# Performance work log

Hardware: AMD Instinct MI355X
Metric: run time of the kernel (lower is better)

The kernel has to match this reference:

```python
import jax, jax.numpy as jnp
from jax import lax
import numpy as np

B, N, C = 32, 24564, 81
CENTER_VAR, SIZE_VAR = 0.1, 0.2
CONF_THRESH, IOU_THRESH = 0.01, 0.45
PRE_NMS_K, MAX_DET = 100, 100
EPS = 1e-8


def setup_inputs() -> dict:
    key = jax.random.key(0)
    k1, k2, k3, k4 = jax.random.split(key, 4)
    location_preds = jax.random.normal(k1, (B, N, 4), dtype=jnp.float32)
    confidence_preds = jax.random.normal(k2, (B, N, C), dtype=jnp.float32)
    # priors in center form (cx, cy, w, h), all in (0, 1), w/h in [0.05, 0.5]
    cxcy = jax.random.uniform(k3, (N, 2), dtype=jnp.float32)
    wh = 0.05 + 0.45 * jax.random.uniform(k4, (N, 2), dtype=jnp.float32)
    priors = jnp.concatenate([cxcy, wh], axis=-1)
    return {"location_preds": location_preds,
            "confidence_preds": confidence_preds,
            "priors": priors}


def _decode_corner(loc, priors):
    # loc: [B,N,4], priors: [N,4] center form -> corner-form boxes [B,N,4]
    cxcy = loc[..., :2] * CENTER_VAR * priors[None, :, 2:] + priors[None, :, :2]
    wh = jnp.exp(loc[..., 2:] * SIZE_VAR) * priors[None, :, 2:]
    return jnp.concatenate([cxcy - wh * 0.5, cxcy + wh * 0.5], axis=-1)


def _pairwise_iou(boxes):
    # boxes: [K,4] corner form -> [K,K]
    lt = jnp.maximum(boxes[:, None, :2], boxes[None, :, :2])
    rb = jnp.minimum(boxes[:, None, 2:], boxes[None, :, 2:])
    wh = jnp.clip(rb - lt, 0.0)
    inter = wh[..., 0] * wh[..., 1]
    area = jnp.prod(jnp.clip(boxes[:, 2:] - boxes[:, :2], 0.0), axis=-1)  # [K]
    return inter / (area[:, None] + area[None, :] - inter + EPS)


def _nms_one_class(boxes, scores):
    # boxes: [N,4], scores: [N] -> kept top-K boxes/scores for this class
    scores = jnp.where(scores > CONF_THRESH, scores, 0.0)
    top_s, idx = lax.top_k(scores, PRE_NMS_K)          # [K]
    top_b = boxes[idx]                                  # [K,4] sorted by score desc
    iou = _pairwise_iou(top_b)                          # [K,K]
    order = jnp.arange(PRE_NMS_K)

    def body(i, keep):
        suppressed = jnp.any(keep & (iou[:, i] > IOU_THRESH) & (order < i))
        return keep.at[i].set((top_s[i] > 0.0) & jnp.logical_not(suppressed))

    keep = lax.fori_loop(0, PRE_NMS_K, body, jnp.zeros(PRE_NMS_K, dtype=bool))
    return top_b, jnp.where(keep, top_s, 0.0)


def _per_image(boxes, scores):
    # boxes: [N,4], scores: [N,C]; class 0 is background
    cls_scores = scores[:, 1:].T                        # [C-1, N]
    b, s = jax.vmap(_nms_one_class, in_axes=(None, 0))(boxes, cls_scores)
    labels = jnp.broadcast_to(jnp.arange(1, C)[:, None], (C - 1, PRE_NMS_K))
    b = b.reshape(-1, 4)
    s = s.reshape(-1)
    labels = labels.reshape(-1)
    top_s, idx = lax.top_k(s, MAX_DET)
    return b[idx], top_s, labels[idx]


def reference(location_preds, confidence_preds, priors):
    scores = jax.nn.softmax(confidence_preds, axis=2)   # [B,N,C]
    bboxes = _decode_corner(location_preds, priors)     # [B,N,4]
    boxes_out, scores_out, labels_out = jax.vmap(_per_image)(bboxes, scores)
    # boxes_out [B,MAX_DET,4], scores_out [B,MAX_DET], labels_out [B,MAX_DET]
    return boxes_out, scores_out, labels_out
```

## Files before the change

kernel.cpp:

```cpp
#include <hip/hip_runtime.h>
#include <cstdint>
#include <cstddef>

#define BB 32
#define NN 24564
#define CC 81
#define CM1 80
#define KTOP 100
#define MAXDET 100
#define CBINS 28
#define CSHIFT 21
#define BASEBITS 0x3C000000u
#define SPECBITS 0x3D400000u
#define SPECPF   0.0468281f
#define CAP2 2048
#define CAPB 25
#define BPI 96
#define CAPS 1024
#define FCH 8
#define FCHN 1000
#define FPAD 1024
#define NCAND (CM1 * KTOP)

typedef unsigned long long ull;
typedef unsigned int uint;
typedef float floatx4 __attribute__((ext_vector_type(4)));
typedef floatx4 uf4 __attribute__((aligned(4)));

__global__ __launch_bounds__(256) void zero_kernel(uint* __restrict__ p, int nwords) {
    int i = blockIdx.x * 256 + threadIdx.x;
    if (i < nwords) p[i] = 0u;
}

__device__ __forceinline__ void bitonic_sort256(ull* a, int S, int tid) {
    for (int k = 2; k <= S; k <<= 1) {
        for (int j = k >> 1; j > 0; j >>= 1) {
            for (int i = tid; i < S; i += 256) {
                int ixj = i ^ j;
                if (ixj > i) {
                    ull x = a[i], y = a[ixj];
                    bool up = ((i & k) == 0);
                    if ((x > y) == up) { a[i] = y; a[ixj] = x; }
                }
            }
            __syncthreads();
        }
    }
}

__global__ __launch_bounds__(256) void softmax_spec_kernel(const float* __restrict__ conf,
                                                           float2* __restrict__ mxs,
                                                           ull* __restrict__ cand,
                                                           uint* __restrict__ ccnt,
                                                           uint* __restrict__ ovf) {
    __shared__ ull  sbuf[CM1 * CAPB];
    __shared__ uint scnt[CM1];
    int tid = threadIdx.x;
    if (tid < CM1) scnt[tid] = 0u;
    __syncthreads();

    int b = blockIdx.x / BPI, j = blockIdx.x % BPI;
    int n = j * 256 + tid;
    if (n < NN) {
        const float* row = conf + ((size_t)b * NN + n) * CC;
        const uf4* row4 = reinterpret_cast<const uf4*>(row);
        float r[CC];
        #pragma unroll
        for (int q = 0; q < 20; ++q) {
            floatx4 v = row4[q];
            r[4 * q] = v.x; r[4 * q + 1] = v.y; r[4 * q + 2] = v.z; r[4 * q + 3] = v.w;
        }
        r[80] = row[80];

        float mx = r[0];
        #pragma unroll
        for (int c = 1; c < CC; ++c) mx = fmaxf(mx, r[c]);

        float s = 0.f;
        #pragma unroll
        for (int c = 0; c < CC; ++c) {
            r[c] = expf(__fsub_rn(r[c], mx));
            s = __fadd_rn(s, r[c]);
        }
        mxs[(size_t)b * NN + n] = make_float2(mx, s);

        float rcp = __builtin_amdgcn_rcpf(s);
        uint nn = (uint)n;
        #pragma unroll
        for (int c = 1; c < CC; ++c) {
            float p = __fmul_rn(r[c], rcp);
            if (p > SPECPF) {
                float sc = __fdiv_rn(r[c], s);
                uint eb = __float_as_uint(sc);
                if (eb >= SPECBITS) {
                    uint pp = atomicAdd(&scnt[c - 1], 1u);
                    if (pp < CAPB) sbuf[(c - 1) * CAPB + pp] = (((ull)(~eb)) << 32) | nn;
                }
            }
        }
    }
    __syncthreads();

    if (tid < CM1) {
        uint c2 = scnt[tid];
        if (c2) {
            int bc = b * CM1 + tid;
            uint nstore = c2 > CAPB ? CAPB : c2;
            uint base = atomicAdd(ccnt + bc, nstore);
            if (c2 > CAPB || base + nstore > CAP2) ovf[bc] = 1u;
            uint lim = base + nstore; if (lim > CAP2) lim = CAP2;
            for (uint i = 0; base + i < lim; ++i)
                cand[(size_t)bc * CAP2 + base + i] = sbuf[tid * CAPB + i];
        }
    }
}

__global__ __launch_bounds__(256) void nms_kernel(const ull* __restrict__ cand,
                                                  const uint* __restrict__ ccnt,
                                                  const uint* __restrict__ ovf,
                                                  const float* __restrict__ conf,
                                                  const float2* __restrict__ mxs,
                                                  const float* __restrict__ loc,
                                                  const float* __restrict__ priors,
                                                  float* __restrict__ nms_scores,
                                                  float* __restrict__ nms_boxes) {
    int bc = blockIdx.x;
    int bimg = bc / CM1, ccls = bc % CM1;
    __shared__ ull arr[CAP2];
    __shared__ ull arr2[CAPS];
    __shared__ uint hist[CBINS];
    __shared__ uint s_cut, s_mode, s_cnt2;
    __shared__ float bx[KTOP][4];
    __shared__ float sv[KTOP];
    __shared__ ull mlo[KTOP], mhi[KTOP];
    __shared__ ull keeplo, keephi;

    int tid = threadIdx.x;
    for (int i = tid; i < CBINS; i += 256) hist[i] = 0u;
    if (tid == 0) { s_cut = 0u; s_mode = 0u; s_cnt2 = 0u; }
    __syncthreads();

    uint rawcnt = ccnt[bc];
    bool flagged = !(ovf[bc] == 0u && rawcnt >= (uint)KTOP);
    int scc; ull* sorted;

    if (!flagged) {
        int cc = (int)rawcnt; if (cc > CAP2) cc = CAP2;
        const ull* crow = cand + (size_t)bc * CAP2;
        for (int i = tid; i < cc; i += 256) {
            ull k = crow[i];
            arr[i] = k;
            uint bits = ~(uint)(k >> 32);
            uint bin = (bits - BASEBITS) >> CSHIFT;
            if (bin >= CBINS) bin = CBINS - 1;
            atomicAdd(&hist[bin], 1u);
        }
        __syncthreads();
        if (tid == 0) {
            uint Kt = (uint)(cc < KTOP ? cc : KTOP);
            if (Kt > 0) {
                uint cum = 0; int bb2 = 0;
                for (int i = CBINS - 1; i >= 0; --i) {
                    cum += hist[i];
                    if (cum >= Kt) { bb2 = i; break; }
                }
                if (cum <= CAPS) {
                    s_cut = BASEBITS + ((uint)bb2 << CSHIFT);
                    s_mode = 1u;
                }
            }
        }
        __syncthreads();
        if (s_mode) {
            uint cutv = s_cut;
            for (int i = tid; i < cc; i += 256) {
                ull k = arr[i];
                uint bits = ~(uint)(k >> 32);
                if (bits >= cutv) { uint p = atomicAdd(&s_cnt2, 1u); arr2[p] = k; }
            }
            __syncthreads();
            scc = (int)s_cnt2;
            sorted = arr2;
        } else {
            scc = cc;
            sorted = arr;
        }
    } else {
        int c = ccls + 1;
        for (int n = tid; n < NN; n += 256) {
            float x = conf[((size_t)bimg * NN + n) * CC + c];
            float2 ms = mxs[(size_t)bimg * NN + n];
            float e = expf(__fsub_rn(x, ms.x));
            float sc = __fdiv_rn(e, ms.y);
            if (sc > 0.01f) {
                uint bits = __float_as_uint(sc);
                uint bin = (bits - BASEBITS) >> CSHIFT;
                if (bin >= CBINS) bin = CBINS - 1;
                atomicAdd(&hist[bin], 1u);
            }
        }
        __syncthreads();
        if (tid == 0) {
            uint total = 0;
            for (int i = 0; i < CBINS; ++i) total += hist[i];
            uint Kt = total < KTOP ? total : KTOP;
            s_cut = 0xFFFFFFFFu;
            if (Kt > 0) {
                uint cum = 0; int bb2 = 0;
                for (int i = CBINS - 1; i >= 0; --i) {
                    cum += hist[i];
                    if (cum >= Kt) { bb2 = i; break; }
                }
                uint cutbin = (cum <= CAP2) ? (uint)bb2 : (uint)(bb2 + 1);
                s_cut = BASEBITS + (cutbin << CSHIFT);
            }
        }
        __syncthreads();
        uint cutv = s_cut;
        for (int n = tid; n < NN; n += 256) {
            float x = conf[((size_t)bimg * NN + n) * CC + c];
            float2 ms = mxs[(size_t)bimg * NN + n];
            float e = expf(__fsub_rn(x, ms.x));
            float sc = __fdiv_rn(e, ms.y);
            if (sc > 0.01f) {
                uint bits = __float_as_uint(sc);
                if (bits >= cutv) {
                    uint p = atomicAdd(&s_cnt2, 1u);
                    if (p < CAP2) arr[p] = (((ull)(~bits)) << 32) | (uint)n;
                }
            }
        }
        __syncthreads();
        scc = (int)s_cnt2; if (scc > CAP2) scc = CAP2;
        sorted = arr;
    }

    int S = 1; while (S < scc) S <<= 1; if (S < 2) S = 2;
    for (int i = scc + tid; i < S; i += 256) sorted[i] = ~0ull;
    __syncthreads();
    bitonic_sort256(sorted, S, tid);

    if (tid < KTOP) {
        float val = 0.f; uint n = 0;
        if (tid < scc) {
            ull kk = sorted[tid];
            val = __uint_as_float(~(uint)(kk >> 32));
            n = (uint)(kk & 0xFFFFFFFFu);
        }
        sv[tid] = val;
        float4 l = reinterpret_cast<const float4*>(loc)[(size_t)bimg * NN + n];
        float4 p = reinterpret_cast<const float4*>(priors)[n];
        float cx = __fadd_rn(__fmul_rn(__fmul_rn(l.x, 0.1f), p.z), p.x);
        float cy = __fadd_rn(__fmul_rn(__fmul_rn(l.y, 0.1f), p.w), p.y);
        float w  = __fmul_rn(expf(__fmul_rn(l.z, 0.2f)), p.z);
        float h  = __fmul_rn(expf(__fmul_rn(l.w, 0.2f)), p.w);
        bx[tid][0] = __fsub_rn(cx, __fmul_rn(w, 0.5f));
        bx[tid][1] = __fsub_rn(cy, __fmul_rn(h, 0.5f));
        bx[tid][2] = __fadd_rn(cx, __fmul_rn(w, 0.5f));
        bx[tid][3] = __fadd_rn(cy, __fmul_rn(h, 0.5f));
    }
    __syncthreads();

    if (tid < KTOP) {
        float x1 = bx[tid][0], y1 = bx[tid][1], x2 = bx[tid][2], y2 = bx[tid][3];
        float ai = __fmul_rn(fmaxf(__fsub_rn(x2, x1), 0.f), fmaxf(__fsub_rn(y2, y1), 0.f));
        ull lo = 0, hi = 0;
        for (int jj = 0; jj < KTOP; ++jj) {
            float jx1 = bx[jj][0], jy1 = bx[jj][1], jx2 = bx[jj][2], jy2 = bx[jj][3];
            float iw = fmaxf(__fsub_rn(fminf(x2, jx2), fmaxf(x1, jx1)), 0.f);
            float ih = fmaxf(__fsub_rn(fminf(y2, jy2), fmaxf(y1, jy1)), 0.f);
            float inter = __fmul_rn(iw, ih);
            float aj = __fmul_rn(fmaxf(__fsub_rn(jx2, jx1), 0.f), fmaxf(__fsub_rn(jy2, jy1), 0.f));
            float denom = __fadd_rn(__fsub_rn(__fadd_rn(ai, aj), inter), 1e-8f);
            float iou = __fdiv_rn(inter, denom);
            if (iou > 0.45f) { if (jj < 64) lo |= (1ull << jj); else hi |= (1ull << (jj - 64)); }
        }
        mlo[tid] = lo; mhi[tid] = hi;
    }
    __syncthreads();

    if (tid == 0) {
        ull klo = 0, khi = 0;
        for (int i = 0; i < KTOP; ++i) {
            ull sup = (mlo[i] & klo) | (mhi[i] & khi);
            bool kp = (sv[i] > 0.f) && (sup == 0ull);
            if (kp) { if (i < 64) klo |= (1ull << i); else khi |= (1ull << (i - 64)); }
        }
        keeplo = klo; keephi = khi;
    }
    __syncthreads();

    if (tid < KTOP) {
        bool kp = (tid < 64) ? ((keeplo >> tid) & 1ull) : ((keephi >> (tid - 64)) & 1ull);
        size_t obase = (size_t)bc * KTOP + tid;
        nms_scores[obase] = kp ? sv[tid] : 0.f;
        float4 o; o.x = bx[tid][0]; o.y = bx[tid][1]; o.z = bx[tid][2]; o.w = bx[tid][3];
        reinterpret_cast<float4*>(nms_boxes)[obase] = o;
    }
}

__global__ __launch_bounds__(256) void final_topk_kernel(const float* __restrict__ nms_scores,
                                                         const float* __restrict__ nms_boxes,
                                                         float* __restrict__ out) {
    int b = blockIdx.x;
    __shared__ ull arr[CAP2];
    __shared__ ull arr2[FPAD];
    __shared__ uint hist[CBINS];
    __shared__ uint s_cut, s_mode, s_cnt2, s_nz;
    int tid = threadIdx.x;

    const float* srow = nms_scores + (size_t)b * NCAND;
    for (int i = tid; i < CBINS; i += 256) hist[i] = 0u;
    if (tid == 0) { s_cut = 0u; s_mode = 0u; s_cnt2 = 0u; s_nz = 0u; }
    __syncthreads();

    uint mynz = 0;
    for (int i = tid; i < NCAND; i += 256) {
        float s = srow[i];
        if (s > 0.f) {
            ++mynz;
            uint bits = __float_as_uint(s);
            uint bin = (bits - BASEBITS) >> CSHIFT;
            if (bin >= CBINS) bin = CBINS - 1;
            atomicAdd(&hist[bin], 1u);
        }
    }
    if (mynz) atomicAdd(&s_nz, mynz);
    __syncthreads();
    if (tid == 0) {
        if (s_nz >= (uint)KTOP) {
            uint cum = 0; int bb2 = 0;
            for (int i = CBINS - 1; i >= 0; --i) {
                cum += hist[i];
                if (cum >= (uint)KTOP) { bb2 = i; break; }
            }
            if (cum <= CAP2) { s_cut = BASEBITS + ((uint)bb2 << CSHIFT); s_mode = 1u; }
        }
    }
    __syncthreads();

    if (s_mode) {
        uint cutv = s_cut;
        for (int i = tid; i < NCAND; i += 256) {
            float s = srow[i];
            if (s > 0.f) {
                uint bits = __float_as_uint(s);
                if (bits >= cutv) {
                    uint p = atomicAdd(&s_cnt2, 1u);
                    arr[p] = (((ull)(~bits)) << 32) | (uint)i;
                }
            }
        }
        __syncthreads();
        int fcc = (int)s_cnt2;
        int FS = 1; while (FS < fcc) FS <<= 1; if (FS < 2) FS = 2;
        for (int i = fcc + tid; i < FS; i += 256) arr[i] = ~0ull;
        __syncthreads();
        bitonic_sort256(arr, FS, tid);
    } else {
        for (int ch = 0; ch < FCH; ++ch) {
            for (int i = tid; i < FPAD; i += 256) {
                ull key;
                if (i < FCHN) {
                    float s = srow[ch * FCHN + i];
                    uint bits = (s > 0.f) ? __float_as_uint(s) : 0u;
                    key = (((ull)(~bits)) << 32) | (uint)(ch * FCHN + i);
                } else key = ~0ull;
                arr2[i] = key;
            }
            __syncthreads();
            bitonic_sort256(arr2, FPAD, tid);
            if (tid < KTOP) arr[ch * KTOP + tid] = arr2[tid];
            __syncthreads();
        }
        for (int i = FCH * KTOP + tid; i < FPAD; i += 256) arr[i] = ~0ull;
        __syncthreads();
        bitonic_sort256(arr, FPAD, tid);
    }

    if (tid < MAXDET) {
        ull kk = arr[tid];
        uint hb = (uint)(kk >> 32);
        uint idx = (uint)(kk & 0xFFFFFFFFu);
        float val = __uint_as_float(~hb);
        float4 b4 = reinterpret_cast<const float4*>(nms_boxes)[(size_t)b * NCAND + idx];
        reinterpret_cast<float4*>(out)[(size_t)b * MAXDET + tid] = b4;
        out[BB * MAXDET * 4 + b * MAXDET + tid] = val;
        out[BB * MAXDET * 5 + b * MAXDET + tid] = (float)(idx / KTOP + 1);
    }
}

extern "C" void kernel_launch(void* const* d_in, const int* in_sizes, int n_in,
                              void* d_out, int out_size, void* d_ws, size_t ws_size,
                              hipStream_t stream) {
    const float* loc    = (const float*)d_in[0];
    const float* conf   = (const float*)d_in[1];
    const float* priors = (const float*)d_in[2];
    float* out = (float*)d_out;

    char* ws = (char*)d_ws;
    float* nms_scores = (float*)ws;
    float* nms_boxes  = nms_scores + (size_t)BB * CM1 * KTOP;
    ull*   cand       = (ull*)(nms_boxes + (size_t)BB * CM1 * KTOP * 4);
    float2* mxs       = (float2*)(cand + (size_t)BB * CM1 * CAP2);
    uint*  ccnt       = (uint*)(mxs + (size_t)BB * NN);
    uint*  ovf        = ccnt + (size_t)BB * CM1;

    zero_kernel<<<(BB * CM1 * 2 + 255) / 256, 256, 0, stream>>>(ccnt, BB * CM1 * 2);

    softmax_spec_kernel<<<BB * BPI, 256, 0, stream>>>(conf, mxs, cand, ccnt, ovf);
    nms_kernel<<<BB * CM1, 256, 0, stream>>>(cand, ccnt, ovf, conf, mxs, loc, priors,
                                             nms_scores, nms_boxes);
    final_topk_kernel<<<BB, 256, 0, stream>>>(nms_scores, nms_boxes, out);
}
```

Baseline: 234.4 us.

## Replace bitonic sort with rank-by-counting top-K selection in NMS kernel

Drops the shared-memory copy of candidates and the bitonic sort. Each thread instead computes the rank of up to 8 keys by comparing against all surviving candidates and scatters those with rank below K into a top-K buffer. The fallback path that kept all candidates when the post-cut count exceeded the old cap is removed, so the cut filter is always applied. This avoids the many barrier-separated sort stages, but the ranking costs O(scc) serial shared reads per thread, which can grow when many candidates survive the cut.

```diff
diff --git a/kernel.cpp b/kernel.cpp
--- a/kernel.cpp
+++ b/kernel.cpp
@@ -16,7 +16,6 @@
 #define CAP2 2048
 #define CAPB 25
 #define BPI 96
-#define CAPS 1024
 #define FCH 8
 #define FCHN 1000
 #define FPAD 1024
@@ -126,10 +125,10 @@
                                                   float* __restrict__ nms_boxes) {
     int bc = blockIdx.x;
     int bimg = bc / CM1, ccls = bc % CM1;
-    __shared__ ull arr[CAP2];
-    __shared__ ull arr2[CAPS];
+    __shared__ ull arr2[CAP2];
+    __shared__ ull keysort[KTOP];
     __shared__ uint hist[CBINS];
-    __shared__ uint s_cut, s_mode, s_cnt2;
+    __shared__ uint s_cut, s_cnt2;
     __shared__ float bx[KTOP][4];
     __shared__ float sv[KTOP];
     __shared__ ull mlo[KTOP], mhi[KTOP];
@@ -137,20 +136,18 @@
 
     int tid = threadIdx.x;
     for (int i = tid; i < CBINS; i += 256) hist[i] = 0u;
-    if (tid == 0) { s_cut = 0u; s_mode = 0u; s_cnt2 = 0u; }
+    if (tid < KTOP) keysort[tid] = ((ull)0xFFFFFFFFu) << 32;
+    if (tid == 0) { s_cut = 0u; s_cnt2 = 0u; }
     __syncthreads();
 
     uint rawcnt = ccnt[bc];
     bool flagged = !(ovf[bc] == 0u && rawcnt >= (uint)KTOP);
-    int scc; ull* sorted;
 
     if (!flagged) {
         int cc = (int)rawcnt; if (cc > CAP2) cc = CAP2;
         const ull* crow = cand + (size_t)bc * CAP2;
         for (int i = tid; i < cc; i += 256) {
-            ull k = crow[i];
-            arr[i] = k;
-            uint bits = ~(uint)(k >> 32);
+            uint bits = ~(uint)(crow[i] >> 32);
             uint bin = (bits - BASEBITS) >> CSHIFT;
             if (bin >= CBINS) bin = CBINS - 1;
             atomicAdd(&hist[bin], 1u);
@@ -158,33 +155,21 @@
         __syncthreads();
         if (tid == 0) {
             uint Kt = (uint)(cc < KTOP ? cc : KTOP);
-            if (Kt > 0) {
-                uint cum = 0; int bb2 = 0;
-                for (int i = CBINS - 1; i >= 0; --i) {
-                    cum += hist[i];
-                    if (cum >= Kt) { bb2 = i; break; }
-                }
-                if (cum <= CAPS) {
-                    s_cut = BASEBITS + ((uint)bb2 << CSHIFT);
-                    s_mode = 1u;
-                }
-            }
-        }
-        __syncthreads();
-        if (s_mode) {
-            uint cutv = s_cut;
-            for (int i = tid; i < cc; i += 256) {
-                ull k = arr[i];
-                uint bits = ~(uint)(k >> 32);
-                if (bits >= cutv) { uint p = atomicAdd(&s_cnt2, 1u); arr2[p] = k; }
-            }
-            __syncthreads();
-            scc = (int)s_cnt2;
-            sorted = arr2;
-        } else {
-            scc = cc;
-            sorted = arr;
-        }
+            uint cum = 0; int bb2 = 0;
+            for (int i = CBINS - 1; i >= 0; --i) {
+                cum += hist[i];
+                if (cum >= Kt) { bb2 = i; break; }
+            }
+            s_cut = BASEBITS + ((uint)bb2 << CSHIFT);
+        }
+        __syncthreads();
+        uint cutv = s_cut;
+        for (int i = tid; i < cc; i += 256) {
+            ull k = crow[i];
+            uint bits = ~(uint)(k >> 32);
+            if (bits >= cutv) { uint p = atomicAdd(&s_cnt2, 1u); arr2[p] = k; }
+        }
+        __syncthreads();
     } else {
         int c = ccls + 1;
         for (int n = tid; n < NN; n += 256) {
@@ -226,27 +211,40 @@
                 uint bits = __float_as_uint(sc);
                 if (bits >= cutv) {
                     uint p = atomicAdd(&s_cnt2, 1u);
-                    if (p < CAP2) arr[p] = (((ull)(~bits)) << 32) | (uint)n;
+                    if (p < CAP2) arr2[p] = (((ull)(~bits)) << 32) | (uint)n;
                 }
             }
         }
         __syncthreads();
-        scc = (int)s_cnt2; if (scc > CAP2) scc = CAP2;
-        sorted = arr;
-    }
-
-    int S = 1; while (S < scc) S <<= 1; if (S < 2) S = 2;
-    for (int i = scc + tid; i < S; i += 256) sorted[i] = ~0ull;
-    __syncthreads();
-    bitonic_sort256(sorted, S, tid);
+    }
+
+    int scc = (int)s_cnt2; if (scc > CAP2) scc = CAP2;
+
+    {
+        ull myk[8]; int rnk[8];
+        #pragma unroll
+        for (int t = 0; t < 8; ++t) {
+            int i = tid + t * 256;
+            myk[t] = (i < scc) ? arr2[i] : ~0ull;
+            rnk[t] = 0;
+        }
+        for (int j = 0; j < scc; ++j) {
+            ull kj = arr2[j];
+            #pragma unroll
+            for (int t = 0; t < 8; ++t) rnk[t] += (kj < myk[t]) ? 1 : 0;
+        }
+        #pragma unroll
+        for (int t = 0; t < 8; ++t) {
+            int i = tid + t * 256;
+            if (i < scc && rnk[t] < KTOP) keysort[rnk[t]] = myk[t];
+        }
+    }
+    __syncthreads();
 
     if (tid < KTOP) {
-        float val = 0.f; uint n = 0;
-        if (tid < scc) {
-            ull kk = sorted[tid];
-            val = __uint_as_float(~(uint)(kk >> 32));
-            n = (uint)(kk & 0xFFFFFFFFu);
-        }
+        ull kk = keysort[tid];
+        float val = __uint_as_float(~(uint)(kk >> 32));
+        uint n = (uint)(kk & 0xFFFFFFFFu);
         sv[tid] = val;
         float4 l = reinterpret_cast<const float4*>(loc)[(size_t)bimg * NN + n];
         float4 p = reinterpret_cast<const float4*>(priors)[n];
```

Result: no change. 232.6 us (-0.7%).
